# Kernel optimization log

Measured on AMD Instinct MI355X. Metric: run time of the kernel, lower is better.

The kernel has to match this reference:

```python
import jax, jax.numpy as jnp
import numpy as np

B, T, N_EMBD = 4, 2048, 1024
NUM_EXPERTS, TOP_K = 8, 2
N_CITIES = 4
LIN = N_EMBD + 32 + N_EMBD // 4 + N_EMBD // 4 + N_EMBD // 8 + N_EMBD // 8  # 1824


def setup_inputs() -> dict:
    key = jax.random.key(0)
    ks = jax.random.split(key, 12)
    s = 0.02  # init std as in _init_weights
    return {
        "x": jax.random.normal(ks[0], (B, T, N_EMBD), jnp.float32),
        "delta_t_info": jax.random.normal(ks[1], (B, T, N_EMBD // 4), jnp.float32),
        "delta_dis_info": jax.random.normal(ks[2], (B, T, N_EMBD // 4), jnp.float32),
        "delta_rg_info": jax.random.normal(ks[3], (B, T, N_EMBD // 8), jnp.float32),
        "delta_entropy_info": jax.random.normal(ks[4], (B, T, N_EMBD // 8), jnp.float32),
        "city_embeddings": jax.random.normal(ks[5], (N_CITIES, 32), jnp.float32),
        "Wg": jax.random.normal(ks[6], (LIN, NUM_EXPERTS), jnp.float32) * s,
        "bg": jnp.zeros((NUM_EXPERTS,), jnp.float32),
        "W1": jax.random.normal(ks[7], (NUM_EXPERTS, N_EMBD, 4 * N_EMBD), jnp.float32) * s,
        "b1": jnp.zeros((NUM_EXPERTS, 4 * N_EMBD), jnp.float32),
        "W2": jax.random.normal(ks[8], (NUM_EXPERTS, 4 * N_EMBD, N_EMBD), jnp.float32) * s,
        "b2": jnp.zeros((NUM_EXPERTS, N_EMBD), jnp.float32),
        "city_index": 1,
    }


def _moe(x, dt, dd, drg, de, city_embeddings, Wg, bg, W1, b1, W2, b2, city_index):
    b, t, _ = x.shape
    city = jnp.broadcast_to(city_embeddings[city_index], (b, t, 32))
    feats = jnp.concatenate([x, city, dt, dd, drg, de], axis=-1)  # [B,T,LIN]
    logits = jnp.einsum("btl,le->bte", feats, Wg) + bg            # eval mode: no noise
    gate1 = jax.nn.softmax(logits, axis=-1)
    _, topi = jax.lax.top_k(logits, TOP_K)                        # [B,T,k]
    # mask of top-k experts per token; scatter(-inf elsewhere) + softmax
    mask = jax.nn.one_hot(topi, NUM_EXPERTS, dtype=jnp.float32).sum(axis=-2) > 0
    sparse_logits = jnp.where(mask, logits, -jnp.inf)
    gates = jax.nn.softmax(sparse_logits, axis=-1)                # zeros outside top-k
    out = jnp.zeros_like(x)
    for e in range(NUM_EXPERTS):  # fixed small expert set
        h = jax.nn.gelu(jnp.einsum("btc,ch->bth", x, W1[e]) + b1[e], approximate=True)
        y = jnp.einsum("bth,hc->btc", h, W2[e]) + b2[e]
        out = out + gates[..., e:e + 1] * y  # gate is exactly 0 for non-topk tokens
    return out, gate1


def reference(x, delta_t_info, delta_dis_info, delta_rg_info, delta_entropy_info,
              city_embeddings, Wg, bg, W1, b1, W2, b2, city_index):
    return _moe(x, delta_t_info, delta_dis_info, delta_rg_info, delta_entropy_info,
                city_embeddings, Wg, bg, W1, b1, W2, b2, city_index)
```

## Files before the change

### kernel.cpp

```cpp
#include <hip/hip_runtime.h>
#include <hip/hip_bf16.h>
#include <stdint.h>

#define NTOK 8192
#define DEMB 1024
#define HDIM 4096
#define NEXP 8
#define LINF 1824
#define MAXPAD 18432

typedef __attribute__((ext_vector_type(8))) __bf16 bf16x8;
typedef __attribute__((ext_vector_type(4))) __bf16 bf16x4v;
typedef __attribute__((ext_vector_type(4))) float f32x4;

__device__ __forceinline__ void gload_lds16(const void* g, void* l) {
  __builtin_amdgcn_global_load_lds(
      (const __attribute__((address_space(1))) void*)g,
      (__attribute__((address_space(3))) void*)l, 16, 0, 0);
}

__device__ __forceinline__ float dot4(float4 a, float4 b) {
  return a.x*b.x + a.y*b.y + a.z*b.z + a.w*b.w;
}

__global__ void __launch_bounds__(256) k_logits(
    const float* __restrict__ x, const float* __restrict__ dt,
    const float* __restrict__ dd, const float* __restrict__ drg,
    const float* __restrict__ de, const float* __restrict__ city,
    const float* __restrict__ Wg, const float* __restrict__ bg,
    const int* __restrict__ city_index,
    float* __restrict__ gate1, int* __restrict__ top_i, float2* __restrict__ top_g,
    __bf16* __restrict__ xb)
{
  __shared__ float WgT[NEXP * LINF];
  const int tid = threadIdx.x;
  const float4* Wg4 = (const float4*)Wg;
  for (int i = tid; i < LINF * NEXP / 4; i += 256) {
    float4 v = Wg4[i];
    int e0 = (i & 1) * 4, f = i >> 1;
    WgT[(e0+0)*LINF + f] = v.x; WgT[(e0+1)*LINF + f] = v.y;
    WgT[(e0+2)*LINF + f] = v.z; WgT[(e0+3)*LINF + f] = v.w;
  }
  __syncthreads();

  const int wave = tid >> 6, lane = tid & 63;
  const int ci = city_index[0];
  const float4* city4 = (const float4*)(city + ci*32);
  const float4 z4 = {0.f, 0.f, 0.f, 0.f};

  #pragma unroll
  for (int k = 0; k < 4; ++k) {
    const int t = blockIdx.x*16 + wave*4 + k;
    const float4* x4 = (const float4*)x + (size_t)t*256;
    float4 xv0 = x4[lane], xv1 = x4[64+lane], xv2 = x4[128+lane], xv3 = x4[192+lane];

    {
      bf16x4v* xrow = (bf16x4v*)(xb + (size_t)t*1024);
      bf16x4v o0, o1, o2, o3;
      o0[0]=(__bf16)xv0.x; o0[1]=(__bf16)xv0.y; o0[2]=(__bf16)xv0.z; o0[3]=(__bf16)xv0.w;
      o1[0]=(__bf16)xv1.x; o1[1]=(__bf16)xv1.y; o1[2]=(__bf16)xv1.z; o1[3]=(__bf16)xv1.w;
      o2[0]=(__bf16)xv2.x; o2[1]=(__bf16)xv2.y; o2[2]=(__bf16)xv2.z; o2[3]=(__bf16)xv2.w;
      o3[0]=(__bf16)xv3.x; o3[1]=(__bf16)xv3.y; o3[2]=(__bf16)xv3.z; o3[3]=(__bf16)xv3.w;
      xrow[lane] = o0; xrow[64+lane] = o1; xrow[128+lane] = o2; xrow[192+lane] = o3;
    }

    float4 cv = (lane < 8) ? city4[lane] : z4;
    float4 tv = ((const float4*)dt)[(size_t)t*64 + lane];
    float4 dv = ((const float4*)dd)[(size_t)t*64 + lane];
    float4 rv = z4, ev = z4;
    if (lane < 32) {
      rv = ((const float4*)drg)[(size_t)t*32 + lane];
      ev = ((const float4*)de )[(size_t)t*32 + lane];
    }
    float a[8];
    const int l8 = lane & 7, l32 = lane & 31;
    #pragma unroll
    for (int e = 0; e < 8; ++e) {
      const float4* W = (const float4*)(WgT + e*LINF);
      float s = dot4(xv0, W[lane]) + dot4(xv1, W[64+lane])
              + dot4(xv2, W[128+lane]) + dot4(xv3, W[192+lane]);
      s += dot4(cv, W[256 + l8]);
      s += dot4(tv, W[264 + lane]) + dot4(dv, W[328 + lane]);
      s += dot4(rv, W[392 + l32]) + dot4(ev, W[424 + l32]);
      a[e] = s;
    }
    #pragma unroll
    for (int off = 32; off > 0; off >>= 1)
      #pragma unroll
      for (int e = 0; e < 8; ++e) a[e] += __shfl_xor(a[e], off);

    float lg[8];
    #pragma unroll
    for (int e = 0; e < 8; ++e) lg[e] = a[e] + bg[e];
    float mx = lg[0];
    #pragma unroll
    for (int e = 1; e < 8; ++e) mx = fmaxf(mx, lg[e]);
    float ex[8]; float s = 0.f;
    #pragma unroll
    for (int e = 0; e < 8; ++e) { ex[e] = expf(lg[e] - mx); s += ex[e]; }
    int i1 = 0; float l1 = lg[0];
    #pragma unroll
    for (int e = 1; e < 8; ++e) if (lg[e] > l1) { l1 = lg[e]; i1 = e; }
    int i2 = -1; float l2 = -1e30f;
    #pragma unroll
    for (int e = 0; e < 8; ++e) if (e != i1 && lg[e] > l2) { l2 = lg[e]; i2 = e; }
    float e2 = expf(l2 - l1);

    if (lane == 0) {
      float inv = 1.f / s;
      float4 o0 = { ex[0]*inv, ex[1]*inv, ex[2]*inv, ex[3]*inv };
      float4 o1 = { ex[4]*inv, ex[5]*inv, ex[6]*inv, ex[7]*inv };
      float4* gp = (float4*)(gate1 + (size_t)t*8);
      gp[0] = o0; gp[1] = o1;
      top_i[t] = i1 | (i2 << 4);
      float2 g = { 1.f / (1.f + e2), e2 / (1.f + e2) };
      top_g[t] = g;
    }
  }
}

__global__ void __launch_bounds__(256) k_build(
    const int* __restrict__ top_i, const float2* __restrict__ top_g,
    int* __restrict__ counts, int* __restrict__ ex_tok, float* __restrict__ ex_gate,
    int2* __restrict__ ppos)
{
  __shared__ int lcnt[8], lbase[8];
  const int tid = threadIdx.x;
  if (tid < 8) lcnt[tid] = 0;
  __syncthreads();
  const int t = blockIdx.x*256 + tid;
  const int ti = top_i[t];
  const int i1 = ti & 15, i2 = ti >> 4;
  const float2 g = top_g[t];
  int p1 = atomicAdd(&lcnt[i1], 1);
  int p2 = atomicAdd(&lcnt[i2], 1);
  __syncthreads();
  if (tid < 8) lbase[tid] = atomicAdd(&counts[tid], lcnt[tid]);
  __syncthreads();
  int s1 = lbase[i1] + p1; ex_tok[i1*NTOK+s1] = t; ex_gate[i1*NTOK+s1] = g.x;
  int s2 = lbase[i2] + p2; ex_tok[i2*NTOK+s2] = t; ex_gate[i2*NTOK+s2] = g.y;
  int2 pp = { i1 | (s1 << 3), i2 | (s2 << 3) };
  ppos[t] = pp;
}

__global__ void k_finalize(const int* __restrict__ counts, int* __restrict__ seg) {
  if (threadIdx.x == 0 && blockIdx.x == 0) {
    int s = 0;
    for (int e = 0; e < 8; ++e) { seg[e] = s; s += (counts[e] + 255) & ~255; }
    seg[8] = s;
  }
}

template<int RDIM, int CDIM>
__global__ void __launch_bounds__(256) k_tconv(
    const float* __restrict__ W, __bf16* __restrict__ WT)
{
  const int e  = blockIdx.z;
  const int c0 = blockIdx.x * 64, r0 = blockIdx.y * 64;
  __shared__ float tb[64 * 65];
  const float* src = W  + (size_t)e * RDIM * CDIM + (size_t)r0 * CDIM + c0;
  __bf16*      dst = WT + (size_t)e * RDIM * CDIM + (size_t)c0 * RDIM + r0;
  const int tx = threadIdx.x & 15, ty = threadIdx.x >> 4;
  #pragma unroll
  for (int i = 0; i < 4; ++i) {
    int r = ty + i*16;
    float4 v = *(const float4*)(src + (size_t)r*CDIM + tx*4);
    tb[(tx*4+0)*65 + r] = v.x; tb[(tx*4+1)*65 + r] = v.y;
    tb[(tx*4+2)*65 + r] = v.z; tb[(tx*4+3)*65 + r] = v.w;
  }
  __syncthreads();
  const int sg = threadIdx.x & 7, dr8 = threadIdx.x >> 3;
  #pragma unroll
  for (int i = 0; i < 2; ++i) {
    int d = dr8 + i*32;
    const float* row = tb + d*65 + sg*8;
    bf16x8 o;
    #pragma unroll
    for (int j = 0; j < 8; ++j) o[j] = (__bf16)row[j];
    *(bf16x8*)(dst + (size_t)d*RDIM + sg*8) = o;
  }
}

template<int KDIM, int KFULL, int NDIM, bool G1>
__global__ void __launch_bounds__(512, 2) k_moe_gemm8(
    const __bf16* __restrict__ Abase, const __bf16* __restrict__ WT,
    const float* __restrict__ bias,
    const int* __restrict__ seg, const int* __restrict__ counts,
    const int* __restrict__ ex_tok,
    int chunk0, __bf16* __restrict__ dstbuf)
{
  constexpr int NT = KDIM / 64;
  const int nx = gridDim.x, ny = gridDim.y, nz = gridDim.z;
  const int total = nx * ny * nz;
  int flat;
  if (G1) flat = blockIdx.x + nx * blockIdx.y;
  else    flat = blockIdx.y + ny * (blockIdx.x + nx * blockIdx.z);
  { int q = total >> 3, r = total & 7; int xcd = flat & 7, idx = flat >> 3;
    flat = (xcd < r ? xcd*(q+1) : r*(q+1) + (xcd-r)*q) + idx; }
  int bx, by, bz;
  if (G1) { bx = flat % nx; by = flat / nx; bz = 0; }
  else    { by = flat % ny; int f2 = flat / ny; bx = f2 % nx; bz = f2 / nx; }

  const int segtot = seg[8];
  const int row0 = chunk0 + bx * 256;
  if (row0 >= segtot) return;
  int e = 0;
  #pragma unroll
  for (int qq = 1; qq < 8; ++qq) if (row0 >= seg[qq]) e = qq;
  const int cnt = counts[e], sege = seg[e];
  const int n0 = by * 256;
  const int kbase = bz * KDIM;

  __shared__ __align__(16) char smem[131072];

  const int tid = threadIdx.x;
  const int wid = tid >> 6, lane = tid & 63;
  const int wm = wid >> 2, wn = wid & 3;
  const int l15 = lane & 15, l4 = lane >> 4;
  const __bf16* Bsrc = WT + (size_t)e * NDIM * KFULL;

  float bv[4];
  if (G1) {
    #pragma unroll
    for (int N = 0; N < 4; ++N)
      bv[N] = bias[(size_t)e*NDIM + n0 + wn*64 + N*16 + l15];
    asm volatile("" :: "v"(bv[0]), "v"(bv[1]), "v"(bv[2]), "v"(bv[3]));
  }

  const __bf16* sp[4][2];
  #pragma unroll
  for (int j = 0; j < 2; ++j) {
    int g = j*512 + tid;
    int sl = g >> 3;
    int kb = (g & 7) ^ (sl & 7);
    #pragma unroll
    for (int mh = 0; mh < 2; ++mh) {
      int wms = (sl >> 6) & 1, rs = sl & 63;
      int R = wms*128 + mh*64 + rs;
      int arow;
      if (G1) { int lr = row0 + R - sege; arow = (lr < cnt) ? ex_tok[e*NTOK + lr] : 0; }
      else    { arow = row0 + R - chunk0; }
      sp[mh][j] = Abase + (size_t)arow * KFULL + kbase + kb*8;
    }
    #pragma unroll
    for (int nh = 0; nh < 2; ++nh) {
      int wns = (sl >> 5) & 3, rs = sl & 31;
      int C = wns*64 + nh*32 + rs;
      sp[2+nh][j] = Bsrc + (size_t)(n0 + C) * KFULL + kbase + kb*8;
    }
  }

  int xo[2];
  #pragma unroll
  for (int kk = 0; kk < 2; ++kk) xo[kk] = (((kk*4 + l4) ^ (l15 & 7)) * 16);
  int arb[4], brb[2];
  #pragma unroll
  for (int m = 0; m < 4; ++m) arb[m] = (wm*64 + m*16 + l15) * 128;
  #pragma unroll
  for (int n = 0; n < 2; ++n) brb[n] = 32768 + (wn*32 + n*16 + l15) * 128;

  auto ISSUE = [&](int h, int tt) {
    char* b = smem + (tt & 1) * 65536 + h * 16384;
    gload_lds16(sp[h][0] + tt*64, b + tid*16);
    gload_lds16(sp[h][1] + tt*64, b + 8192 + tid*16);
  };

  f32x4 acc[8][4] = {};

  ISSUE(0,0); ISSUE(2,0); ISSUE(3,0); ISSUE(1,0);
  ISSUE(0,1); ISSUE(2,1); ISSUE(3,1);
  asm volatile("s_waitcnt vmcnt(10)" ::: "memory");
  __builtin_amdgcn_s_barrier();

  for (int t = 0; t < NT; ++t) {
    const char* cb = smem + (t & 1) * 65536;
    const int tc1 = (t+1 < NT) ? t+1 : NT-1;
    const int tc2 = (t+2 < NT) ? t+2 : NT-1;
    bf16x8 af[4][2], bfr[2][2][2];

    #pragma unroll
    for (int m = 0; m < 4; ++m)
      #pragma unroll
      for (int kk = 0; kk < 2; ++kk)
        af[m][kk] = *(const bf16x8*)(cb + arb[m] + xo[kk]);
    #pragma unroll
    for (int n = 0; n < 2; ++n)
      #pragma unroll
      for (int kk = 0; kk < 2; ++kk)
        bfr[0][n][kk] = *(const bf16x8*)(cb + brb[n] + xo[kk]);
    ISSUE(1, tc1);
    __builtin_amdgcn_s_barrier();
    __builtin_amdgcn_s_setprio(1);
    #pragma unroll
    for (int m = 0; m < 4; ++m)
      #pragma unroll
      for (int n = 0; n < 2; ++n)
        #pragma unroll
        for (int kk = 0; kk < 2; ++kk)
          acc[m][n] = __builtin_amdgcn_mfma_f32_16x16x32_bf16(af[m][kk], bfr[0][n][kk], acc[m][n], 0, 0, 0);
    __builtin_amdgcn_s_setprio(0);
    asm volatile("s_waitcnt vmcnt(10)" ::: "memory");
    __builtin_amdgcn_s_barrier();

    #pragma unroll
    for (int n = 0; n < 2; ++n)
      #pragma unroll
      for (int kk = 0; kk < 2; ++kk)
        bfr[1][n][kk] = *(const bf16x8*)(cb + 16384 + brb[n] + xo[kk]);
    ISSUE(0, tc2);
    __builtin_amdgcn_s_barrier();
    __builtin_amdgcn_s_setprio(1);
    #pragma unroll
    for (int m = 0; m < 4; ++m)
      #pragma unroll
      for (int n = 0; n < 2; ++n)
        #pragma unroll
        for (int kk = 0; kk < 2; ++kk)
          acc[m][2+n] = __builtin_amdgcn_mfma_f32_16x16x32_bf16(af[m][kk], bfr[1][n][kk], acc[m][2+n], 0, 0, 0);
    __builtin_amdgcn_s_setprio(0);
    asm volatile("s_waitcnt vmcnt(10)" ::: "memory");
    __builtin_amdgcn_s_barrier();

    #pragma unroll
    for (int m = 0; m < 4; ++m)
      #pragma unroll
      for (int kk = 0; kk < 2; ++kk)
        af[m][kk] = *(const bf16x8*)(cb + 16384 + arb[m] + xo[kk]);
    ISSUE(2, tc2);
    __builtin_amdgcn_s_barrier();
    __builtin_amdgcn_s_setprio(1);
    #pragma unroll
    for (int m = 0; m < 4; ++m)
      #pragma unroll
      for (int n = 0; n < 2; ++n)
        #pragma unroll
        for (int kk = 0; kk < 2; ++kk)
          acc[4+m][n] = __builtin_amdgcn_mfma_f32_16x16x32_bf16(af[m][kk], bfr[0][n][kk], acc[4+m][n], 0, 0, 0);
    __builtin_amdgcn_s_setprio(0);
    asm volatile("s_waitcnt vmcnt(10)" ::: "memory");
    __builtin_amdgcn_s_barrier();

    ISSUE(3, tc2);
    __builtin_amdgcn_s_barrier();
    __builtin_amdgcn_s_setprio(1);
    #pragma unroll
    for (int m = 0; m < 4; ++m)
      #pragma unroll
      for (int n = 0; n < 2; ++n)
        #pragma unroll
        for (int kk = 0; kk < 2; ++kk)
          acc[4+m][2+n] = __builtin_amdgcn_mfma_f32_16x16x32_bf16(af[m][kk], bfr[1][n][kk], acc[4+m][2+n], 0, 0, 0);
    __builtin_amdgcn_s_setprio(0);
    asm volatile("s_waitcnt vmcnt(10)" ::: "memory");
    __builtin_amdgcn_s_barrier();
  }

  __syncthreads();
  __bf16* Cl = (__bf16*)smem;
  #pragma unroll
  for (int M = 0; M < 8; ++M) {
    #pragma unroll
    for (int N = 0; N < 4; ++N) {
      #pragma unroll
      for (int r2 = 0; r2 < 4; ++r2) {
        float v = acc[M][N][r2];
        if (G1) {
          v += bv[N];
          float z = 2.302208f * (v + 0.044715f * v * v * v);
          v = v / (1.f + exp2f(-z));
        }
        Cl[(wm*128 + M*16 + l4*4 + r2)*256 + wn*64 + N*16 + l15] = (__bf16)v;
      }
    }
  }
  __syncthreads();
  const int drow0 = G1 ? (row0 - chunk0) : row0;
  __bf16* dst = dstbuf + (G1 ? (size_t)0 : (size_t)bz * MAXPAD * NDIM);
  #pragma unroll
  for (int it = 0; it < 16; ++it) {
    int idx2 = it*512 + tid;
    int rr = idx2 >> 5, c8 = (idx2 & 31) * 8;
    *(bf16x8*)(dst + (size_t)(drow0 + rr)*NDIM + n0 + c8) =
        *(const bf16x8*)(Cl + rr*256 + c8);
  }
}

__global__ void __launch_bounds__(256) k_combine(
    const __bf16* __restrict__ pbuf, const int2* __restrict__ ppos,
    const float2* __restrict__ top_g, const int* __restrict__ seg,
    const float* __restrict__ b2, float* __restrict__ out)
{
  const int t = blockIdx.x, tid = threadIdx.x;
  const int2 pp = ppos[t];
  const float2 g = top_g[t];
  const int e1 = pp.x & 7, i1 = pp.x >> 3;
  const int e2 = pp.y & 7, i2 = pp.y >> 3;
  const size_t r1 = (size_t)(seg[e1] + i1) * DEMB;
  const size_t r2 = (size_t)(seg[e2] + i2) * DEMB;
  const int c = tid * 4;
  float4 ba = *(const float4*)(b2 + (size_t)e1*DEMB + c);
  float4 bb = *(const float4*)(b2 + (size_t)e2*DEMB + c);
  float s1x = ba.x, s1y = ba.y, s1z = ba.z, s1w = ba.w;
  float s2x = bb.x, s2y = bb.y, s2z = bb.z, s2w = bb.w;
  #pragma unroll
  for (int p = 0; p < 4; ++p) {
    const __bf16* pb = pbuf + (size_t)p * MAXPAD * DEMB;
    bf16x4v a = *(const bf16x4v*)(pb + r1 + c);
    bf16x4v b = *(const bf16x4v*)(pb + r2 + c);
    s1x += (float)a[0]; s1y += (float)a[1]; s1z += (float)a[2]; s1w += (float)a[3];
    s2x += (float)b[0]; s2y += (float)b[1]; s2z += (float)b[2]; s2w += (float)b[3];
  }
  float4 o;
  o.x = g.x*s1x + g.y*s2x;
  o.y = g.x*s1y + g.y*s2y;
  o.z = g.x*s1z + g.y*s2z;
  o.w = g.x*s1w + g.y*s2w;
  *(float4*)(out + (size_t)t*DEMB + c) = o;
}

extern "C" void kernel_launch(void* const* d_in, const int* in_sizes, int n_in,
                              void* d_out, int out_size, void* d_ws, size_t ws_size,
                              hipStream_t stream)
{
  const float* x   = (const float*)d_in[0];
  const float* dt  = (const float*)d_in[1];
  const float* dd  = (const float*)d_in[2];
  const float* drg = (const float*)d_in[3];
  const float* de  = (const float*)d_in[4];
  const float* city= (const float*)d_in[5];
  const float* Wg  = (const float*)d_in[6];
  const float* bg  = (const float*)d_in[7];
  const float* W1  = (const float*)d_in[8];
  const float* b1  = (const float*)d_in[9];
  const float* W2  = (const float*)d_in[10];
  const float* b2  = (const float*)d_in[11];
  const int* city_index = (const int*)d_in[12];

  float* out   = (float*)d_out;
  float* gate1 = out + (size_t)NTOK * DEMB;

  char* p = (char*)d_ws;
  int*    counts  = (int*)p;      p += 256;
  int*    seg     = (int*)p;      p += 256;
  int*    top_i   = (int*)p;      p += (size_t)NTOK*4;
  float2* top_g   = (float2*)p;   p += (size_t)NTOK*8;
  int2*   ppos    = (int2*)p;     p += (size_t)NTOK*8;
  int*    ex_tok  = (int*)p;      p += (size_t)NTOK*NEXP*4;
  float*  ex_gate = (float*)p;    p += (size_t)NTOK*NEXP*4;
  __bf16* xb      = (__bf16*)p;   p += (size_t)NTOK*DEMB*2;
  __bf16* W1T     = (__bf16*)p;   p += (size_t)NEXP*DEMB*HDIM*2;
  __bf16* W2T     = (__bf16*)p;   p += (size_t)NEXP*DEMB*HDIM*2;
  __bf16* pbuf    = (__bf16*)p;   p += (size_t)4*MAXPAD*DEMB*2;
  __bf16* hbuf    = (__bf16*)p;

  size_t fixed = (size_t)(p - (char*)d_ws);
  int CH = MAXPAD;
  while (CH > 0 && fixed + (size_t)CH * HDIM * 2 > ws_size) CH -= 256;
  if (CH <= 0) return;
  int nch = (MAXPAD + CH - 1) / CH;

  (void)hipMemsetAsync(counts, 0, 64, stream);

  k_tconv<DEMB, HDIM><<<dim3(HDIM/64, DEMB/64, NEXP), 256, 0, stream>>>(W1, W1T);
  k_tconv<HDIM, DEMB><<<dim3(DEMB/64, HDIM/64, NEXP), 256, 0, stream>>>(W2, W2T);

  k_logits<<<NTOK/16, 256, 0, stream>>>(x, dt, dd, drg, de, city, Wg, bg,
                                        city_index, gate1, top_i, top_g, xb);
  k_build<<<NTOK/256, 256, 0, stream>>>(top_i, top_g, counts, ex_tok, ex_gate, ppos);
  k_finalize<<<1, 64, 0, stream>>>(counts, seg);

  for (int c = 0; c < nch; ++c) {
    k_moe_gemm8<1024, 1024, HDIM, true><<<dim3(CH/256, HDIM/256, 1), 512, 0, stream>>>(
        xb, W1T, b1, seg, counts, ex_tok, c*CH, hbuf);
    k_moe_gemm8<1024, 4096, DEMB, false><<<dim3(CH/256, DEMB/256, 4), 512, 0, stream>>>(
        hbuf, W2T, b2, seg, counts, ex_tok, c*CH, pbuf);
  }
  k_combine<<<NTOK, 256, 0, stream>>>(pbuf, ppos, top_g, seg, b2, out);
}
```

Baseline: 525.2 us.

## Shrink MoE GEMM tiles to 128x128 with simple double-buffered loop

Replaces the 256x256, 8-wave MoE GEMM with its staged 4-phase prefetch schedule by a 128x128, 4-wave kernel that uses a plain double buffer and a full vmcnt(0) wait each K-step. The second GEMM's split-K drops from 4 to 2, which halves the partial buffer and the combine reads. The smaller tiles give more blocks and less LDS per block, but they lower arithmetic intensity per tile. The simpler pipeline also exposes more global-load latency.

```diff
diff --git a/kernel.cpp b/kernel.cpp
--- a/kernel.cpp
+++ b/kernel.cpp
@@ -182,7 +182,7 @@
 }
 
 template<int KDIM, int KFULL, int NDIM, bool G1>
-__global__ void __launch_bounds__(512, 2) k_moe_gemm8(
+__global__ void __launch_bounds__(256, 2) k_moe_gemm(
     const __bf16* __restrict__ Abase, const __bf16* __restrict__ WT,
     const float* __restrict__ bias,
     const int* __restrict__ seg, const int* __restrict__ counts,
@@ -202,20 +202,20 @@
   else    { by = flat % ny; int f2 = flat / ny; bx = f2 % nx; bz = f2 / nx; }
 
   const int segtot = seg[8];
-  const int row0 = chunk0 + bx * 256;
+  const int row0 = chunk0 + bx * 128;
   if (row0 >= segtot) return;
   int e = 0;
   #pragma unroll
   for (int qq = 1; qq < 8; ++qq) if (row0 >= seg[qq]) e = qq;
   const int cnt = counts[e], sege = seg[e];
-  const int n0 = by * 256;
+  const int n0 = by * 128;
   const int kbase = bz * KDIM;
 
-  __shared__ __align__(16) char smem[131072];
+  __shared__ __align__(16) char smem[65536];
 
   const int tid = threadIdx.x;
   const int wid = tid >> 6, lane = tid & 63;
-  const int wm = wid >> 2, wn = wid & 3;
+  const int wm = wid >> 1, wn = wid & 1;
   const int l15 = lane & 15, l4 = lane >> 4;
   const __bf16* Bsrc = WT + (size_t)e * NDIM * KFULL;
 
@@ -230,13 +230,12 @@
   const __bf16* sp[4][2];
   #pragma unroll
   for (int j = 0; j < 2; ++j) {
-    int g = j*512 + tid;
+    int g = j*256 + tid;
     int sl = g >> 3;
     int kb = (g & 7) ^ (sl & 7);
     #pragma unroll
     for (int mh = 0; mh < 2; ++mh) {
-      int wms = (sl >> 6) & 1, rs = sl & 63;
-      int R = wms*128 + mh*64 + rs;
+      int R = mh*64 + sl;
       int arow;
       if (G1) { int lr = row0 + R - sege; arow = (lr < cnt) ? ex_tok[e*NTOK + lr] : 0; }
       else    { arow = row0 + R - chunk0; }
@@ -244,8 +243,7 @@
     }
     #pragma unroll
     for (int nh = 0; nh < 2; ++nh) {
-      int wns = (sl >> 5) & 3, rs = sl & 31;
-      int C = wns*64 + nh*32 + rs;
+      int C = nh*64 + sl;
       sp[2+nh][j] = Bsrc + (size_t)(n0 + C) * KFULL + kbase + kb*8;
     }
   }
@@ -253,112 +251,56 @@
   int xo[2];
   #pragma unroll
   for (int kk = 0; kk < 2; ++kk) xo[kk] = (((kk*4 + l4) ^ (l15 & 7)) * 16);
-  int arb[4], brb[2];
-  #pragma unroll
-  for (int m = 0; m < 4; ++m) arb[m] = (wm*64 + m*16 + l15) * 128;
-  #pragma unroll
-  for (int n = 0; n < 2; ++n) brb[n] = 32768 + (wn*32 + n*16 + l15) * 128;
+  int arb[4], brb[4];
+  #pragma unroll
+  for (int m = 0; m < 4; ++m) arb[m] = wm*8192 + (m*16 + l15) * 128;
+  #pragma unroll
+  for (int n = 0; n < 4; ++n) brb[n] = 16384 + wn*8192 + (n*16 + l15) * 128;
 
   auto ISSUE = [&](int h, int tt) {
-    char* b = smem + (tt & 1) * 65536 + h * 16384;
+    char* b = smem + (tt & 1) * 32768 + h * 8192;
     gload_lds16(sp[h][0] + tt*64, b + tid*16);
-    gload_lds16(sp[h][1] + tt*64, b + 8192 + tid*16);
+    gload_lds16(sp[h][1] + tt*64, b + 256*16 + tid*16);
   };
 
-  f32x4 acc[8][4] = {};
-
-  ISSUE(0,0); ISSUE(2,0); ISSUE(3,0); ISSUE(1,0);
-  ISSUE(0,1); ISSUE(2,1); ISSUE(3,1);
-  asm volatile("s_waitcnt vmcnt(10)" ::: "memory");
+  f32x4 acc[4][4] = {};
+
+  ISSUE(0,0); ISSUE(1,0); ISSUE(2,0); ISSUE(3,0);
+  asm volatile("s_waitcnt vmcnt(0)" ::: "memory");
   __builtin_amdgcn_s_barrier();
 
   for (int t = 0; t < NT; ++t) {
-    const char* cb = smem + (t & 1) * 65536;
-    const int tc1 = (t+1 < NT) ? t+1 : NT-1;
-    const int tc2 = (t+2 < NT) ? t+2 : NT-1;
-    bf16x8 af[4][2], bfr[2][2][2];
-
+    const char* cb = smem + (t & 1) * 32768;
+    if (t + 1 < NT) {
+      ISSUE(0, t+1); ISSUE(1, t+1); ISSUE(2, t+1); ISSUE(3, t+1);
+    }
+    bf16x8 af[4][2], bfv[4][2];
     #pragma unroll
     for (int m = 0; m < 4; ++m)
       #pragma unroll
       for (int kk = 0; kk < 2; ++kk)
         af[m][kk] = *(const bf16x8*)(cb + arb[m] + xo[kk]);
     #pragma unroll
-    for (int n = 0; n < 2; ++n)
+    for (int n = 0; n < 4; ++n)
       #pragma unroll
       for (int kk = 0; kk < 2; ++kk)
-        bfr[0][n][kk] = *(const bf16x8*)(cb + brb[n] + xo[kk]);
-    ISSUE(1, tc1);
-    __builtin_amdgcn_s_barrier();
+        bfv[n][kk] = *(const bf16x8*)(cb + brb[n] + xo[kk]);
     __builtin_amdgcn_s_setprio(1);
     #pragma unroll
     for (int m = 0; m < 4; ++m)
       #pragma unroll
-      for (int n = 0; n < 2; ++n)
+      for (int n = 0; n < 4; ++n)
         #pragma unroll
         for (int kk = 0; kk < 2; ++kk)
-          acc[m][n] = __builtin_amdgcn_mfma_f32_16x16x32_bf16(af[m][kk], bfr[0][n][kk], acc[m][n], 0, 0, 0);
+          acc[m][n] = __builtin_amdgcn_mfma_f32_16x16x32_bf16(af[m][kk], bfv[n][kk], acc[m][n], 0, 0, 0);
     __builtin_amdgcn_s_setprio(0);
-    asm volatile("s_waitcnt vmcnt(10)" ::: "memory");
+    asm volatile("s_waitcnt vmcnt(0)" ::: "memory");
     __builtin_amdgcn_s_barrier();
-
-    #pragma unroll
-    for (int n = 0; n < 2; ++n)
-      #pragma unroll
-      for (int kk = 0; kk < 2; ++kk)
-        bfr[1][n][kk] = *(const bf16x8*)(cb + 16384 + brb[n] + xo[kk]);
-    ISSUE(0, tc2);
-    __builtin_amdgcn_s_barrier();
-    __builtin_amdgcn_s_setprio(1);
-    #pragma unroll
-    for (int m = 0; m < 4; ++m)
-      #pragma unroll
-      for (int n = 0; n < 2; ++n)
-        #pragma unroll
-        for (int kk = 0; kk < 2; ++kk)
-          acc[m][2+n] = __builtin_amdgcn_mfma_f32_16x16x32_bf16(af[m][kk], bfr[1][n][kk], acc[m][2+n], 0, 0, 0);
-    __builtin_amdgcn_s_setprio(0);
-    asm volatile("s_waitcnt vmcnt(10)" ::: "memory");
-    __builtin_amdgcn_s_barrier();
-
-    #pragma unroll
-    for (int m = 0; m < 4; ++m)
-      #pragma unroll
-      for (int kk = 0; kk < 2; ++kk)
-        af[m][kk] = *(const bf16x8*)(cb + 16384 + arb[m] + xo[kk]);
-    ISSUE(2, tc2);
-    __builtin_amdgcn_s_barrier();
-    __builtin_amdgcn_s_setprio(1);
-    #pragma unroll
-    for (int m = 0; m < 4; ++m)
-      #pragma unroll
-      for (int n = 0; n < 2; ++n)
-        #pragma unroll
-        for (int kk = 0; kk < 2; ++kk)
-          acc[4+m][n] = __builtin_amdgcn_mfma_f32_16x16x32_bf16(af[m][kk], bfr[0][n][kk], acc[4+m][n], 0, 0, 0);
-    __builtin_amdgcn_s_setprio(0);
-    asm volatile("s_waitcnt vmcnt(10)" ::: "memory");
-    __builtin_amdgcn_s_barrier();
-
-    ISSUE(3, tc2);
-    __builtin_amdgcn_s_barrier();
-    __builtin_amdgcn_s_setprio(1);
-    #pragma unroll
-    for (int m = 0; m < 4; ++m)
-      #pragma unroll
-      for (int n = 0; n < 2; ++n)
-        #pragma unroll
-        for (int kk = 0; kk < 2; ++kk)
-          acc[4+m][2+n] = __builtin_amdgcn_mfma_f32_16x16x32_bf16(af[m][kk], bfr[1][n][kk], acc[4+m][2+n], 0, 0, 0);
-    __builtin_amdgcn_s_setprio(0);
-    asm volatile("s_waitcnt vmcnt(10)" ::: "memory");
-    __builtin_amdgcn_s_barrier();
-  }
-
-  __syncthreads();
+  }
+
   __bf16* Cl = (__bf16*)smem;
   #pragma unroll
-  for (int M = 0; M < 8; ++M) {
+  for (int M = 0; M < 4; ++M) {
     #pragma unroll
     for (int N = 0; N < 4; ++N) {
       #pragma unroll
@@ -369,7 +311,7 @@
           float z = 2.302208f * (v + 0.044715f * v * v * v);
           v = v / (1.f + exp2f(-z));
         }
-        Cl[(wm*128 + M*16 + l4*4 + r2)*256 + wn*64 + N*16 + l15] = (__bf16)v;
+        Cl[(wm*64 + M*16 + l4*4 + r2)*128 + wn*64 + N*16 + l15] = (__bf16)v;
       }
     }
   }
@@ -377,11 +319,11 @@
   const int drow0 = G1 ? (row0 - chunk0) : row0;
   __bf16* dst = dstbuf + (G1 ? (size_t)0 : (size_t)bz * MAXPAD * NDIM);
   #pragma unroll
-  for (int it = 0; it < 16; ++it) {
-    int idx2 = it*512 + tid;
-    int rr = idx2 >> 5, c8 = (idx2 & 31) * 8;
+  for (int it = 0; it < 8; ++it) {
+    int idx2 = it*256 + tid;
+    int rr = idx2 >> 4, c8 = (idx2 & 15) * 8;
     *(bf16x8*)(dst + (size_t)(drow0 + rr)*NDIM + n0 + c8) =
-        *(const bf16x8*)(Cl + rr*256 + c8);
+        *(const bf16x8*)(Cl + rr*128 + c8);
   }
 }
 
@@ -403,7 +345,7 @@
   float s1x = ba.x, s1y = ba.y, s1z = ba.z, s1w = ba.w;
   float s2x = bb.x, s2y = bb.y, s2z = bb.z, s2w = bb.w;
   #pragma unroll
-  for (int p = 0; p < 4; ++p) {
+  for (int p = 0; p < 2; ++p) {
     const __bf16* pb = pbuf + (size_t)p * MAXPAD * DEMB;
     bf16x4v a = *(const bf16x4v*)(pb + r1 + c);
     bf16x4v b = *(const bf16x4v*)(pb + r2 + c);
@@ -450,7 +392,7 @@
   __bf16* xb      = (__bf16*)p;   p += (size_t)NTOK*DEMB*2;
   __bf16* W1T     = (__bf16*)p;   p += (size_t)NEXP*DEMB*HDIM*2;
   __bf16* W2T     = (__bf16*)p;   p += (size_t)NEXP*DEMB*HDIM*2;
-  __bf16* pbuf    = (__bf16*)p;   p += (size_t)4*MAXPAD*DEMB*2;
+  __bf16* pbuf    = (__bf16*)p;   p += (size_t)2*MAXPAD*DEMB*2;
   __bf16* hbuf    = (__bf16*)p;
 
   size_t fixed = (size_t)(p - (char*)d_ws);
@@ -470,9 +412,9 @@
   k_finalize<<<1, 64, 0, stream>>>(counts, seg);
 
   for (int c = 0; c < nch; ++c) {
-    k_moe_gemm8<1024, 1024, HDIM, true><<<dim3(CH/256, HDIM/256, 1), 512, 0, stream>>>(
+    k_moe_gemm<1024, 1024, HDIM, true><<<dim3(CH/128, HDIM/128, 1), 256, 0, stream>>>(
         xb, W1T, b1, seg, counts, ex_tok, c*CH, hbuf);
-    k_moe_gemm8<1024, 4096, DEMB, false><<<dim3(CH/256, DEMB/256, 4), 512, 0, stream>>>(
+    k_moe_gemm<2048, 4096, DEMB, false><<<dim3(CH/128, DEMB/128, 2), 256, 0, stream>>>(
         hbuf, W2T, b2, seg, counts, ex_tok, c*CH, pbuf);
   }
   k_combine<<<NTOK, 256, 0, stream>>>(pbuf, ppos, top_g, seg, b2, out);
```

New measurement: 562.0 us. 7.0% more time.
